# Optimization experiments

Hardware: AMD Instinct MI355X
Metric: run time of the kernel (lower is better)

## Reference

```python
import jax, jax.numpy as jnp
import numpy as np
import math

C = 256
K = 64
STAGE_NUM = 3
UNFOLD_SIZES = (1, 3, 5)


def _l2norm(t, axis):
    return t / (1e-6 + jnp.linalg.norm(t, axis=axis, keepdims=True))


def setup_inputs() -> dict:
    key = jax.random.key(0)
    k0, k1, k2 = jax.random.split(key, 3)
    b, h, w = 4, 64, 64
    x = jax.random.normal(k0, (b, C, h, w), dtype=jnp.float32)
    mu0 = jax.random.normal(k1, (1, C, K), dtype=jnp.float32) * math.sqrt(2.0 / K)
    mu0 = _l2norm(mu0, axis=1)  # matches buffer init: normal_(0, sqrt(2/k)) then l2norm over c
    w_scalar = jnp.array(1.0, dtype=jnp.float32)
    # convcat: Conv2d(3c, c, 1); init std = sqrt(2 / (1*1*out_channels)) = sqrt(2/c)
    w_cat = jax.random.normal(k2, (C, 3 * C), dtype=jnp.float32) * math.sqrt(2.0 / C)
    b_cat = jnp.zeros((C,), dtype=jnp.float32)
    return {"x": x, "mu0": mu0, "w": w_scalar, "w_cat": w_cat, "b_cat": b_cat}


def _mwi_forward(x, mu0, w, w_cat, b_cat):
    b, c, h, wd = x.shape
    k = mu0.shape[2]
    mu = jnp.broadcast_to(mu0, (b, c, k))
    feats = []
    for s in UNFOLD_SIZES:
        p = (s - 1) // 2
        xp = jnp.pad(x, ((0, 0), (0, 0), (p, p), (p, p)))
        # im2col: (b, c, s*s, h, w), kernel positions row-major -> matches torch F.unfold then view(b,c,-1)
        patches = jnp.stack([xp[:, :, i:i + h, j:j + wd] for i in range(s) for j in range(s)], axis=2)
        ux = patches.reshape(b, c, s * s * h * wd)  # (b, c, N)
        z = None
        for _ in range(STAGE_NUM):  # EM iterations (no_grad in original)
            z = jax.nn.softmax(jnp.einsum('bcn,bck->bnk', ux, mu), axis=2)  # E-step
            z_ = z / (1e-6 + z.sum(axis=1, keepdims=True))
            mu = _l2norm(jnp.einsum('bcn,bnk->bck', ux, z_), axis=1)  # M-step
        mu = jax.lax.stop_gradient(mu)
        z = jax.lax.stop_gradient(z)
        zf = jnp.einsum('bck,bnk->bcn', mu, z)  # reconstruction (b, c, N)
        zf = zf.reshape(b, c, s, s, h, wd)
        # col2im (F.fold): overlap-add of kernel positions
        out = jnp.zeros((b, c, h + 2 * p, wd + 2 * p), dtype=x.dtype)
        for i in range(s):
            for j in range(s):
                out = out.at[:, :, i:i + h, j:j + wd].add(zf[:, :, i, j])
        feats.append(out[:, :, p:p + h, p:p + wd])
    cat = jnp.concatenate(feats, axis=1)  # (b, 3c, h, w)
    u = jnp.einsum('bihw,oi->bohw', cat, w_cat) + b_cat[None, :, None, None]
    out = jax.nn.relu(u * w + x)
    return out, mu


def reference(x, mu0, w, w_cat, b_cat):
    return _mwi_forward(x, mu0, w, w_cat, b_cat)
```

## Files before the change

kernel.cpp:

```cpp
#include <hip/hip_runtime.h>

typedef float f32x4 __attribute__((ext_vector_type(4)));
typedef short bf16x8 __attribute__((ext_vector_type(8)));
typedef unsigned short u16;
typedef u16 u16x8 __attribute__((ext_vector_type(8)));
typedef unsigned int u32;

#define B 4
#define C 256
#define K 64
#define NN 4096
#define W3C 768
#define CP 264
#define SP 72

__device__ __forceinline__ u16 bf_hi(float f) {
    unsigned u = __float_as_uint(f);
    u += 0x7FFFu + ((u >> 16) & 1u);
    return (u16)(u >> 16);
}
__device__ __forceinline__ float bf_f(u16 s) { return __uint_as_float(((unsigned)s) << 16); }

__global__ void k_prep(const float* __restrict__ x, const float* __restrict__ mu0,
                       const float* __restrict__ w_cat,
                       u16* __restrict__ xch, u16* __restrict__ xcl,
                       u16* __restrict__ wch, u16* __restrict__ wcl,
                       u16* __restrict__ muth, u16* __restrict__ mutl) {
    int blk = blockIdx.x, tid = threadIdx.x;
    if (blk < 2048) {
        int i = blk * 256 + tid;
        const float4* s4 = (const float4*)(x + (size_t)i * 8);
        float4 a = s4[0], bq = s4[1];
        float v[8] = {a.x, a.y, a.z, a.w, bq.x, bq.y, bq.z, bq.w};
        u16x8 hv, lv;
        #pragma unroll
        for (int j = 0; j < 8; j++) { u16 hh = bf_hi(v[j]); hv[j] = hh; lv[j] = bf_hi(v[j] - bf_f(hh)); }
        *(u16x8*)(xch + (size_t)i * 8) = hv;
        *(u16x8*)(xcl + (size_t)i * 8) = lv;
    } else if (blk < 2144) {
        int i = (blk - 2048) * 256 + tid;
        const float4* s4 = (const float4*)(w_cat + (size_t)i * 8);
        float4 a = s4[0], bq = s4[1];
        float v[8] = {a.x, a.y, a.z, a.w, bq.x, bq.y, bq.z, bq.w};
        u16x8 hv, lv;
        #pragma unroll
        for (int j = 0; j < 8; j++) { u16 hh = bf_hi(v[j]); hv[j] = hh; lv[j] = bf_hi(v[j] - bf_f(hh)); }
        *(u16x8*)(wch + (size_t)i * 8) = hv;
        *(u16x8*)(wcl + (size_t)i * 8) = lv;
    } else {
        int g = (blk - 2144) * 256 + tid;
        int kq = (g >> 8) & 63, cq = g & 255;
        float v = mu0[cq * K + kq];
        u16 hh = bf_hi(v);
        muth[g] = hh;
        mutl[g] = bf_hi(v - bf_f(hh));
    }
}

__global__ __launch_bounds__(256) void k_em(
        const u16* __restrict__ xch, const u16* __restrict__ xcl,
        const u16* __restrict__ muth, const u16* __restrict__ mutl,
        float* __restrict__ tpart, float* __restrict__ dpart,
        u16* __restrict__ sig_out, int pv, int write_sig)
{
    extern __shared__ char smem[];
    u16* sxh = (u16*)smem;
    u16* sxl = sxh + 64 * CP;
    u16* smh = sxl + 64 * CP;
    u16* sml = smh + 64 * CP;
    u16* sTh = sml + 64 * CP;
    u16* sTl = sTh + 64 * SP;
    float* redf = (float*)(sTl + 64 * SP);

    const int ch = blockIdx.x, b = blockIdx.y, tid = threadIdx.x;
    const int n0 = ch * 64;

    {
        int p2 = tid & 127, h = tid >> 7;
        #pragma unroll
        for (int nc = 0; nc < 4; nc++) {
            int nrow = h * 32 + nc * 8;
            u16x8 a0h = *(const u16x8*)&xch[((size_t)(b * C + 2 * p2)) * NN + n0 + nrow];
            u16x8 a1h = *(const u16x8*)&xch[((size_t)(b * C + 2 * p2 + 1)) * NN + n0 + nrow];
            u16x8 a0l = *(const u16x8*)&xcl[((size_t)(b * C + 2 * p2)) * NN + n0 + nrow];
            u16x8 a1l = *(const u16x8*)&xcl[((size_t)(b * C + 2 * p2 + 1)) * NN + n0 + nrow];
            #pragma unroll
            for (int j = 0; j < 8; j++) {
                *(u32*)&sxh[(nrow + j) * CP + 2 * p2] = (u32)a0h[j] | ((u32)a1h[j] << 16);
                *(u32*)&sxl[(nrow + j) * CP + 2 * p2] = (u32)a0l[j] | ((u32)a1l[j] << 16);
            }
        }
    }
    {
        size_t mbase = ((size_t)(b * K)) * C;
        for (int t = tid; t < 2048; t += 256) {
            int r = t >> 5, cof = (t & 31) * 8;
            *(u16x8*)&smh[r * CP + cof] = *(const u16x8*)&muth[mbase + (size_t)r * C + cof];
            *(u16x8*)&sml[r * CP + cof] = *(const u16x8*)&mutl[mbase + (size_t)r * C + cof];
        }
    }
    __syncthreads();

    const int wid = tid >> 6, l = tid & 63, lg = l >> 4, lr = l & 15;
    f32x4 z4 = {0.f, 0.f, 0.f, 0.f};

    f32x4 acc[4] = {z4, z4, z4, z4};
    for (int cc = 0; cc < 8; cc++) {
        int co = cc * 32 + lg * 8;
        bf16x8 Ah = *(bf16x8*)&sxh[(wid * 16 + lr) * CP + co];
        bf16x8 Al = *(bf16x8*)&sxl[(wid * 16 + lr) * CP + co];
        #pragma unroll
        for (int kt = 0; kt < 4; kt++) {
            bf16x8 Bh = *(bf16x8*)&smh[(kt * 16 + lr) * CP + co];
            bf16x8 Bl = *(bf16x8*)&sml[(kt * 16 + lr) * CP + co];
            acc[kt] = __builtin_amdgcn_mfma_f32_16x16x32_bf16(Ah, Bh, acc[kt], 0, 0, 0);
            acc[kt] = __builtin_amdgcn_mfma_f32_16x16x32_bf16(Al, Bh, acc[kt], 0, 0, 0);
            acc[kt] = __builtin_amdgcn_mfma_f32_16x16x32_bf16(Ah, Bl, acc[kt], 0, 0, 0);
        }
    }

    float swv[4][4];
    float psum[4] = {0.f, 0.f, 0.f, 0.f};
    #pragma unroll
    for (int jj = 0; jj < 4; jj++) {
        int n = n0 + wid * 16 + lg * 4 + jj;
        float v0 = acc[0][jj], v1 = acc[1][jj], v2 = acc[2][jj], v3 = acc[3][jj];
        float m = fmaxf(fmaxf(v0, v1), fmaxf(v2, v3));
        #pragma unroll
        for (int off = 1; off <= 8; off <<= 1) m = fmaxf(m, __shfl_xor(m, off));
        float e0 = __expf(v0 - m), e1 = __expf(v1 - m), e2 = __expf(v2 - m), e3 = __expf(v3 - m);
        float ss = e0 + e1 + e2 + e3;
        #pragma unroll
        for (int off = 1; off <= 8; off <<= 1) ss += __shfl_xor(ss, off);
        int y = n >> 6, xx = n & 63;
        float cnt = (float)((min(pv, y) + min(pv, 63 - y) + 1) * (min(pv, xx) + min(pv, 63 - xx) + 1));
        float sc = cnt / ss;
        swv[jj][0] = e0 * sc; swv[jj][1] = e1 * sc; swv[jj][2] = e2 * sc; swv[jj][3] = e3 * sc;
        #pragma unroll
        for (int kt = 0; kt < 4; kt++) {
            psum[kt] += swv[jj][kt];
            if (write_sig)
                sig_out[((size_t)(b * NN + n)) * K + kt * 16 + lr] = bf_hi(swv[jj][kt]);
        }
    }
    #pragma unroll
    for (int kt = 0; kt < 4; kt++) {
        #pragma unroll
        for (int jp = 0; jp < 2; jp++) {
            float va = swv[2 * jp][kt], vb = swv[2 * jp + 1][kt];
            u16 ha = bf_hi(va), hb = bf_hi(vb);
            u16 la = bf_hi(va - bf_f(ha)), lb = bf_hi(vb - bf_f(hb));
            int col = wid * 16 + lg * 4 + 2 * jp;
            *(u32*)&sTh[(kt * 16 + lr) * SP + col] = (u32)ha | ((u32)hb << 16);
            *(u32*)&sTl[(kt * 16 + lr) * SP + col] = (u32)la | ((u32)lb << 16);
        }
        redf[(kt * 16 + lr) * 17 + wid * 4 + lg] = psum[kt];
    }
    __syncthreads();
    if (tid < 64) {
        float sd = 0.f;
        #pragma unroll
        for (int g2 = 0; g2 < 16; g2++) sd += redf[tid * 17 + g2];
        dpart[((size_t)(b * 64 + ch)) * K + tid] = sd;
    }

    f32x4 macc[16];
    #pragma unroll
    for (int ci = 0; ci < 16; ci++) macc[ci] = z4;
    #pragma unroll
    for (int nn2 = 0; nn2 < 2; nn2++) {
        int no = nn2 * 32 + lg * 8;
        bf16x8 Ah = *(bf16x8*)&sTh[(wid * 16 + lr) * SP + no];
        bf16x8 Al = *(bf16x8*)&sTl[(wid * 16 + lr) * SP + no];
        #pragma unroll
        for (int ci = 0; ci < 16; ci++) {
            size_t go = ((size_t)(b * C + ci * 16 + lr)) * NN + n0 + no;
            bf16x8 Bh = *(const bf16x8*)&xch[go];
            bf16x8 Bl = *(const bf16x8*)&xcl[go];
            macc[ci] = __builtin_amdgcn_mfma_f32_16x16x32_bf16(Ah, Bh, macc[ci], 0, 0, 0);
            macc[ci] = __builtin_amdgcn_mfma_f32_16x16x32_bf16(Al, Bh, macc[ci], 0, 0, 0);
            macc[ci] = __builtin_amdgcn_mfma_f32_16x16x32_bf16(Ah, Bl, macc[ci], 0, 0, 0);
        }
    }
    #pragma unroll
    for (int ci = 0; ci < 16; ci++)
        #pragma unroll
        for (int jj = 0; jj < 4; jj++)
            tpart[((size_t)((b * 64 + ch) * K + wid * 16 + lg * 4 + jj)) * C + ci * 16 + lr]
                = macc[ci][jj];
}

__global__ __launch_bounds__(256) void k_norm(
        const float* __restrict__ tpart, const float* __restrict__ dpart,
        u16* __restrict__ muth, u16* __restrict__ mutl,
        float* __restrict__ out_mu, float dconst) {
    __shared__ float red[256];
    __shared__ float dsh;
    int k = blockIdx.x, b = blockIdx.y, tid = threadIdx.x;
    float dv = 0.f;
    if (tid < 64) dv = dpart[((size_t)(b * 64 + tid)) * K + k];
    #pragma unroll
    for (int off = 1; off <= 32; off <<= 1) dv += __shfl_xor(dv, off);
    if (tid == 0) dsh = dv;
    float tt = 0.f;
    #pragma unroll 8
    for (int chn = 0; chn < 64; chn++)
        tt += tpart[((size_t)((b * 64 + chn) * K + k)) * C + tid];
    red[tid] = tt * tt;
    __syncthreads();
    for (int st = 128; st > 0; st >>= 1) {
        if (tid < st) red[tid] += red[tid + st];
        __syncthreads();
    }
    float d = dconst + dsh;
    float inv = 1.f / (1e-6f * d + sqrtf(red[0]));
    float v = tt * inv;
    u16 hh = bf_hi(v);
    size_t o = ((size_t)(b * K + k)) * C + tid;
    muth[o] = hh;
    mutl[o] = bf_hi(v - bf_f(hh));
    out_mu[((size_t)(b * C + tid)) * K + k] = v;
}

__global__ __launch_bounds__(256) void k_pmat(
        const u16* __restrict__ wch, const u16* __restrict__ wcl,
        const u16* __restrict__ mh_g, const u16* __restrict__ ml_g,
        u16* __restrict__ Pb, int s) {
    int ob = blockIdx.x, b = blockIdx.y;
    int tid = threadIdx.x, w = tid >> 6, l = tid & 63, lg = l >> 4, lr = l & 15;
    f32x4 z4 = {0.f, 0.f, 0.f, 0.f};
    f32x4 acc[4] = {z4, z4, z4, z4};
    int orow = ob * 64 + w * 16 + lr;
    const u16* wbh = wch + (size_t)orow * W3C + s * C;
    const u16* wbl = wcl + (size_t)orow * W3C + s * C;
    for (int cc = 0; cc < 8; cc++) {
        int co = cc * 32 + lg * 8;
        bf16x8 Ah = *(const bf16x8*)&wbh[co];
        bf16x8 Al = *(const bf16x8*)&wbl[co];
        #pragma unroll
        for (int kt = 0; kt < 4; kt++) {
            bf16x8 Bh = *(const bf16x8*)&mh_g[((size_t)(b * K + kt * 16 + lr)) * C + co];
            bf16x8 Bl = *(const bf16x8*)&ml_g[((size_t)(b * K + kt * 16 + lr)) * C + co];
            acc[kt] = __builtin_amdgcn_mfma_f32_16x16x32_bf16(Ah, Bh, acc[kt], 0, 0, 0);
            acc[kt] = __builtin_amdgcn_mfma_f32_16x16x32_bf16(Al, Bh, acc[kt], 0, 0, 0);
            acc[kt] = __builtin_amdgcn_mfma_f32_16x16x32_bf16(Ah, Bl, acc[kt], 0, 0, 0);
        }
    }
    #pragma unroll
    for (int kt = 0; kt < 4; kt++)
        #pragma unroll
        for (int jj = 0; jj < 4; jj++) {
            int o = ob * 64 + w * 16 + lg * 4 + jj;
            Pb[((size_t)((s * B + b) * C + o)) * K + kt * 16 + lr] = bf_hi(acc[kt][jj]);
        }
}

__global__ __launch_bounds__(256) void k_final(
        const u16* __restrict__ sh_g, const u16* __restrict__ Pb,
        const float* __restrict__ x, const float* __restrict__ b_cat,
        const float* __restrict__ wscal, float* __restrict__ out) {
    __shared__ u16 ssig[64 * 72];
    __shared__ u16 sP[64 * 72];
    __shared__ float tbuf[64 * 68];
    int nt = blockIdx.x, ot = blockIdx.y, b = blockIdx.z;
    int n0 = nt * 64, o0 = ot * 64;
    int tid = threadIdx.x, w = tid >> 6, l = tid & 63, lg = l >> 4, lr = l & 15;
    f32x4 z4 = {0.f, 0.f, 0.f, 0.f};
    f32x4 acc[4] = {z4, z4, z4, z4};
    for (int s = 0; s < 3; s++) {
        __syncthreads();
        for (int t = tid; t < 512; t += 256) {
            int r = t >> 3, kc = (t & 7) * 8;
            *(u16x8*)&ssig[r * 72 + kc] =
                *(const u16x8*)&sh_g[(size_t)s * ((size_t)B * NN * K) + ((size_t)(b * NN + n0 + r)) * K + kc];
            *(u16x8*)&sP[r * 72 + kc] =
                *(const u16x8*)&Pb[((size_t)((s * B + b) * C + o0 + r)) * K + kc];
        }
        __syncthreads();
        #pragma unroll
        for (int kk = 0; kk < 2; kk++) {
            int ko = kk * 32 + lg * 8;
            bf16x8 A = *(bf16x8*)&ssig[(w * 16 + lr) * 72 + ko];
            #pragma unroll
            for (int oi = 0; oi < 4; oi++) {
                bf16x8 Bv = *(bf16x8*)&sP[(oi * 16 + lr) * 72 + ko];
                acc[oi] = __builtin_amdgcn_mfma_f32_16x16x32_bf16(A, Bv, acc[oi], 0, 0, 0);
            }
        }
    }
    __syncthreads();
    #pragma unroll
    for (int oi = 0; oi < 4; oi++)
        #pragma unroll
        for (int jj = 0; jj < 4; jj++)
            tbuf[(oi * 16 + lr) * 68 + (w * 16 + lg * 4 + jj)] = acc[oi][jj];
    __syncthreads();
    float wv = wscal[0];
    for (int t = tid; t < 1024; t += 256) {
        int ol = t >> 4, ck = (t & 15) * 4;
        int o = o0 + ol;
        float bc = b_cat[o];
        float4 u4 = *(float4*)&tbuf[ol * 68 + ck];
        size_t base = ((size_t)(b * C + o)) * NN + n0 + ck;
        float4 xv = *(const float4*)&x[base];
        float4 r;
        r.x = fmaxf((u4.x + bc) * wv + xv.x, 0.f);
        r.y = fmaxf((u4.y + bc) * wv + xv.y, 0.f);
        r.z = fmaxf((u4.z + bc) * wv + xv.z, 0.f);
        r.w = fmaxf((u4.w + bc) * wv + xv.w, 0.f);
        *(float4*)&out[base] = r;
    }
}

extern "C" void kernel_launch(void* const* d_in, const int* in_sizes, int n_in,
                              void* d_out, int out_size, void* d_ws, size_t ws_size,
                              hipStream_t stream) {
    const float* x     = (const float*)d_in[0];
    const float* mu0   = (const float*)d_in[1];
    const float* wsc   = (const float*)d_in[2];
    const float* w_cat = (const float*)d_in[3];
    const float* b_cat = (const float*)d_in[4];
    float* out = (float*)d_out;
    char* wsb = (char*)d_ws;

    const size_t SZ_XC   = (size_t)B * C * NN * 2;
    const size_t SZ_MUT  = (size_t)B * K * C * 2;
    const size_t SZ_SIGH = (size_t)3 * B * NN * K * 2;
    const size_t SZ_TP   = (size_t)B * 64 * K * C * 4;
    const size_t SZ_DP   = (size_t)B * 64 * K * 4;
    const size_t SZ_PB   = (size_t)3 * B * C * K * 2;
    const size_t SZ_WC   = (size_t)C * W3C * 2;

    size_t off = 0;
    u16*   xch  = (u16*)(wsb + off); off += SZ_XC;
    u16*   xcl  = (u16*)(wsb + off); off += SZ_XC;
    u16*   muth = (u16*)(wsb + off); off += SZ_MUT;
    u16*   mutl = (u16*)(wsb + off); off += SZ_MUT;
    u16*   sigh = (u16*)(wsb + off); off += SZ_SIGH;
    float* tpart= (float*)(wsb + off); off += SZ_TP;
    float* dpart= (float*)(wsb + off); off += SZ_DP;
    u16*   Pb   = (u16*)(wsb + off); off += SZ_PB;
    u16*   wch  = (u16*)(wsb + off); off += SZ_WC;
    u16*   wcl  = (u16*)(wsb + off); off += SZ_WC;
    float* out_mu = out + (size_t)B * C * NN;

    const int EM_LDS = 4 * 64 * CP * 2 + 2 * 64 * SP * 2 + 1088 * 4;
    hipFuncSetAttribute((const void*)k_em, hipFuncAttributeMaxDynamicSharedMemorySize, EM_LDS);

    k_prep<<<2400, 256, 0, stream>>>(x, mu0, w_cat, xch, xcl, wch, wcl, muth, mutl);

    const int   pvals[3]   = {0, 1, 2};
    const float dconsts[3] = {1e-6f, 1e-6f + 11.9375f, 1e-6f + 59.4375f};

    for (int s = 0; s < 3; s++) {
        u16* shs = sigh + (size_t)s * ((size_t)B * NN * K);
        for (int it = 0; it < 3; it++) {
            k_em<<<dim3(64, B), 256, EM_LDS, stream>>>(xch, xcl, muth, mutl,
                                                       tpart, dpart, shs, pvals[s],
                                                       (it == 2) ? 1 : 0);
            k_norm<<<dim3(K, B), 256, 0, stream>>>(tpart, dpart, muth, mutl,
                                                   out_mu, dconsts[s]);
        }
        k_pmat<<<dim3(4, B), 256, 0, stream>>>(wch, wcl, muth, mutl, Pb, s);
    }
    k_final<<<dim3(64, 4, B), 256, 0, stream>>>(sigh, Pb, x, b_cat, wsc, out);
}
```

Measured before the change: 316.2 us.

## Pre-transpose x to n-major bf16 split and read E-step A operand from global

Adds a transpose kernel that writes the hi/lo bf16 split of x in (b, n, c) layout. The EM kernel then loads its E-step A fragments straight from global memory instead of transposing x into shared memory on every launch. This removes the per-launch LDS transpose and halves the EM kernel's shared memory, which may allow more blocks per CU. The cost is an extra prep kernel, extra workspace, and uncached global loads inside the MFMA loop.

```diff
diff --git a/kernel.cpp b/kernel.cpp
--- a/kernel.cpp
+++ b/kernel.cpp
@@ -57,16 +57,35 @@
     }
 }
 
+__global__ void k_prept(const float* __restrict__ x, u16* __restrict__ th,
+                        u16* __restrict__ tl) {
+    __shared__ float tile[32][33];
+    int b = blockIdx.z, c0 = blockIdx.y * 32, n0 = blockIdx.x * 32;
+    int tx = threadIdx.x, ty = threadIdx.y;
+    #pragma unroll
+    for (int j = 0; j < 4; j++)
+        tile[ty + j * 8][tx] = x[((size_t)(b * C + c0 + ty + j * 8)) * NN + n0 + tx];
+    __syncthreads();
+    #pragma unroll
+    for (int j = 0; j < 4; j++) {
+        int n = n0 + ty + j * 8;
+        float v = tile[tx][ty + j * 8];
+        u16 hh = bf_hi(v);
+        size_t o = ((size_t)(b * NN + n)) * C + c0 + tx;
+        th[o] = hh;
+        tl[o] = bf_hi(v - bf_f(hh));
+    }
+}
+
 __global__ __launch_bounds__(256) void k_em(
+        const u16* __restrict__ xth, const u16* __restrict__ xtl,
         const u16* __restrict__ xch, const u16* __restrict__ xcl,
         const u16* __restrict__ muth, const u16* __restrict__ mutl,
         float* __restrict__ tpart, float* __restrict__ dpart,
         u16* __restrict__ sig_out, int pv, int write_sig)
 {
     extern __shared__ char smem[];
-    u16* sxh = (u16*)smem;
-    u16* sxl = sxh + 64 * CP;
-    u16* smh = sxl + 64 * CP;
+    u16* smh = (u16*)smem;
     u16* sml = smh + 64 * CP;
     u16* sTh = sml + 64 * CP;
     u16* sTl = sTh + 64 * SP;
@@ -75,22 +94,6 @@
     const int ch = blockIdx.x, b = blockIdx.y, tid = threadIdx.x;
     const int n0 = ch * 64;
 
-    {
-        int p2 = tid & 127, h = tid >> 7;
-        #pragma unroll
-        for (int nc = 0; nc < 4; nc++) {
-            int nrow = h * 32 + nc * 8;
-            u16x8 a0h = *(const u16x8*)&xch[((size_t)(b * C + 2 * p2)) * NN + n0 + nrow];
-            u16x8 a1h = *(const u16x8*)&xch[((size_t)(b * C + 2 * p2 + 1)) * NN + n0 + nrow];
-            u16x8 a0l = *(const u16x8*)&xcl[((size_t)(b * C + 2 * p2)) * NN + n0 + nrow];
-            u16x8 a1l = *(const u16x8*)&xcl[((size_t)(b * C + 2 * p2 + 1)) * NN + n0 + nrow];
-            #pragma unroll
-            for (int j = 0; j < 8; j++) {
-                *(u32*)&sxh[(nrow + j) * CP + 2 * p2] = (u32)a0h[j] | ((u32)a1h[j] << 16);
-                *(u32*)&sxl[(nrow + j) * CP + 2 * p2] = (u32)a0l[j] | ((u32)a1l[j] << 16);
-            }
-        }
-    }
     {
         size_t mbase = ((size_t)(b * K)) * C;
         for (int t = tid; t < 2048; t += 256) {
@@ -105,17 +108,21 @@
     f32x4 z4 = {0.f, 0.f, 0.f, 0.f};
 
     f32x4 acc[4] = {z4, z4, z4, z4};
-    for (int cc = 0; cc < 8; cc++) {
-        int co = cc * 32 + lg * 8;
-        bf16x8 Ah = *(bf16x8*)&sxh[(wid * 16 + lr) * CP + co];
-        bf16x8 Al = *(bf16x8*)&sxl[(wid * 16 + lr) * CP + co];
-        #pragma unroll
-        for (int kt = 0; kt < 4; kt++) {
-            bf16x8 Bh = *(bf16x8*)&smh[(kt * 16 + lr) * CP + co];
-            bf16x8 Bl = *(bf16x8*)&sml[(kt * 16 + lr) * CP + co];
-            acc[kt] = __builtin_amdgcn_mfma_f32_16x16x32_bf16(Ah, Bh, acc[kt], 0, 0, 0);
-            acc[kt] = __builtin_amdgcn_mfma_f32_16x16x32_bf16(Al, Bh, acc[kt], 0, 0, 0);
-            acc[kt] = __builtin_amdgcn_mfma_f32_16x16x32_bf16(Ah, Bl, acc[kt], 0, 0, 0);
+    {
+        const u16* xrh = xth + ((size_t)(b * NN + n0 + wid * 16 + lr)) * C;
+        const u16* xrl = xtl + ((size_t)(b * NN + n0 + wid * 16 + lr)) * C;
+        for (int cc = 0; cc < 8; cc++) {
+            int co = cc * 32 + lg * 8;
+            bf16x8 Ah = *(const bf16x8*)&xrh[co];
+            bf16x8 Al = *(const bf16x8*)&xrl[co];
+            #pragma unroll
+            for (int kt = 0; kt < 4; kt++) {
+                bf16x8 Bh = *(bf16x8*)&smh[(kt * 16 + lr) * CP + co];
+                bf16x8 Bl = *(bf16x8*)&sml[(kt * 16 + lr) * CP + co];
+                acc[kt] = __builtin_amdgcn_mfma_f32_16x16x32_bf16(Ah, Bh, acc[kt], 0, 0, 0);
+                acc[kt] = __builtin_amdgcn_mfma_f32_16x16x32_bf16(Al, Bh, acc[kt], 0, 0, 0);
+                acc[kt] = __builtin_amdgcn_mfma_f32_16x16x32_bf16(Ah, Bl, acc[kt], 0, 0, 0);
+            }
         }
     }
 
@@ -323,7 +330,7 @@
     float* out = (float*)d_out;
     char* wsb = (char*)d_ws;
 
-    const size_t SZ_XC   = (size_t)B * C * NN * 2;
+    const size_t SZ_X2   = (size_t)B * C * NN * 2;
     const size_t SZ_MUT  = (size_t)B * K * C * 2;
     const size_t SZ_SIGH = (size_t)3 * B * NN * K * 2;
     const size_t SZ_TP   = (size_t)B * 64 * K * C * 4;
@@ -332,8 +339,10 @@
     const size_t SZ_WC   = (size_t)C * W3C * 2;
 
     size_t off = 0;
-    u16*   xch  = (u16*)(wsb + off); off += SZ_XC;
-    u16*   xcl  = (u16*)(wsb + off); off += SZ_XC;
+    u16*   xch  = (u16*)(wsb + off); off += SZ_X2;
+    u16*   xcl  = (u16*)(wsb + off); off += SZ_X2;
+    u16*   xth  = (u16*)(wsb + off); off += SZ_X2;
+    u16*   xtl  = (u16*)(wsb + off); off += SZ_X2;
     u16*   muth = (u16*)(wsb + off); off += SZ_MUT;
     u16*   mutl = (u16*)(wsb + off); off += SZ_MUT;
     u16*   sigh = (u16*)(wsb + off); off += SZ_SIGH;
@@ -344,10 +353,11 @@
     u16*   wcl  = (u16*)(wsb + off); off += SZ_WC;
     float* out_mu = out + (size_t)B * C * NN;
 
-    const int EM_LDS = 4 * 64 * CP * 2 + 2 * 64 * SP * 2 + 1088 * 4;
+    const int EM_LDS = 2 * 64 * CP * 2 + 2 * 64 * SP * 2 + 1088 * 4;
     hipFuncSetAttribute((const void*)k_em, hipFuncAttributeMaxDynamicSharedMemorySize, EM_LDS);
 
     k_prep<<<2400, 256, 0, stream>>>(x, mu0, w_cat, xch, xcl, wch, wcl, muth, mutl);
+    k_prept<<<dim3(128, 8, B), dim3(32, 8), 0, stream>>>(x, xth, xtl);
 
     const int   pvals[3]   = {0, 1, 2};
     const float dconsts[3] = {1e-6f, 1e-6f + 11.9375f, 1e-6f + 59.4375f};
@@ -355,7 +365,7 @@
     for (int s = 0; s < 3; s++) {
         u16* shs = sigh + (size_t)s * ((size_t)B * NN * K);
         for (int it = 0; it < 3; it++) {
-            k_em<<<dim3(64, B), 256, EM_LDS, stream>>>(xch, xcl, muth, mutl,
+            k_em<<<dim3(64, B), 256, EM_LDS, stream>>>(xth, xtl, xch, xcl, muth, mutl,
                                                        tpart, dpart, shs, pvals[s],
                                                        (it == 2) ? 1 : 0);
             k_norm<<<dim3(K, B), 256, 0, stream>>>(tpart, dpart, muth, mutl,
```

Result: faster. 298.7 us (-5.5%).
